# Kernel tuning notes

Hardware: AMD Instinct MI355X
Metric: run time of the kernel (lower is better)

The kernel has to match this reference:

```python
import jax, jax.numpy as jnp
import numpy as np

N = 8192
IN_DIM = 256
OUT_DIM = 256  # out_dim//num_heads * num_heads == out_dim
EDGE_PROB = 0.01


def setup_inputs() -> dict:
    key = jax.random.key(0)
    k_adj, k_h, k_q, k_k, k_v = jax.random.split(key, 5)
    # Dense 0/1 adjacency mask, multiplied into the score matrix.
    adj = (jax.random.uniform(k_adj, (N, N)) < EDGE_PROB).astype(jnp.float32)
    h = jax.random.normal(k_h, (N, IN_DIM), dtype=jnp.float32)
    # torch nn.Linear stores weight as [out_features, in_features]; no bias (use_bias=False).
    s = 1.0 / np.sqrt(IN_DIM)
    Wq = jax.random.normal(k_q, (OUT_DIM, IN_DIM), dtype=jnp.float32) * s
    Wk = jax.random.normal(k_k, (OUT_DIM, IN_DIM), dtype=jnp.float32) * s
    Wv = jax.random.normal(k_v, (OUT_DIM, IN_DIM), dtype=jnp.float32) * s
    return {"adj": adj, "h": h, "Wq": Wq, "Wk": Wk, "Wv": Wv}


def reference(adj, h, Wq, Wk, Wv):
    # Q_h, K_h, V_h: [N, out_dim]
    Q_h = h @ Wq.T
    K_h = h @ Wk.T
    V_h = h @ Wv.T
    scale = 1.0 / jnp.sqrt(jnp.asarray(h.shape[1], dtype=h.dtype))
    # Scores masked multiplicatively by adjacency (faithful to source: zeros,
    # not -inf, so non-edges still contribute exp(0) after softmax).
    A_tilde = scale * (Q_h @ K_h.T) * adj            # [N, N]
    attention = jax.nn.softmax(A_tilde, axis=1)       # softmax over dim 1
    X_tilde = attention @ V_h                         # [N, out_dim]
    return X_tilde
```

## Files before the change

### kernel.cpp

```cpp
#include <hip/hip_runtime.h>


#define NN  8192
#define DIM 256
#define SCALE 0.0625f
#define CAP 32

typedef __attribute__((ext_vector_type(8))) short short8;
typedef __attribute__((ext_vector_type(4))) float f32x4;
typedef __attribute__((ext_vector_type(4))) unsigned int u32x4;
typedef __attribute__((ext_vector_type(4))) unsigned short u16x4;

__device__ __forceinline__ unsigned short f2bf(float f) {
    union { float f; unsigned u; } v; v.f = f;
    unsigned u = v.u;
    unsigned r = (u + 0x7fffu + ((u >> 16) & 1u)) >> 16;
    return (unsigned short)r;
}
__device__ __forceinline__ float bf2f(unsigned short s) {
    union { unsigned u; float f; } v; v.u = ((unsigned)s) << 16;
    return v.f;
}
__device__ __forceinline__ float dw_lo(unsigned u) {
    union { unsigned u; float f; } v; v.u = u << 16; return v.f;
}
__device__ __forceinline__ float dw_hi(unsigned u) {
    union { unsigned u; float f; } v; v.u = u & 0xffff0000u; return v.f;
}

__global__ __launch_bounds__(256) void prep_kernel(
    const float* __restrict__ h, const float* __restrict__ Wq,
    const float* __restrict__ Wk, const float* __restrict__ Wv,
    unsigned short* __restrict__ h_bf, unsigned short* __restrict__ w_bf)
{
    int b = blockIdx.x, t = threadIdx.x;
    if (b < 2048) {
        int idx = (b * 256 + t) * 4;
        float4 v = *(const float4*)(h + idx);
        ushort4 o; o.x = f2bf(v.x); o.y = f2bf(v.y); o.z = f2bf(v.z); o.w = f2bf(v.w);
        *(ushort4*)(h_bf + idx) = o;
    } else {
        int idx = ((b - 2048) * 256 + t) * 4;
        int w = idx >> 16;
        int offn = idx & 65535;
        const float* src = (w == 0) ? Wq : (w == 1) ? Wk : Wv;
        float4 v = *(const float4*)(src + offn);
        ushort4 o; o.x = f2bf(v.x); o.y = f2bf(v.y); o.z = f2bf(v.z); o.w = f2bf(v.w);
        *(ushort4*)(w_bf + idx) = o;
    }
}

__global__ __launch_bounds__(256) void proj_gemm(
    const unsigned short* __restrict__ h_bf, const unsigned short* __restrict__ w_bf,
    float* __restrict__ Q, unsigned short* __restrict__ Kb, unsigned short* __restrict__ Vb)
{
    __shared__ unsigned short sB[256][40];
    const int mb = blockIdx.x, p = blockIdx.y;
    const unsigned short* W = w_bf + (p << 16);
    const int tid = threadIdx.x, wave = tid >> 6, lane = tid & 63;

    f32x4 acc[16];
#pragma unroll
    for (int f = 0; f < 16; ++f) acc[f] = (f32x4)(0.0f);

    const int arow = mb * 64 + wave * 16 + (lane & 15);
    const int ko   = (lane >> 4) * 8;

    for (int kk = 0; kk < 256; kk += 32) {
        __syncthreads();
        {
            const uint4* src = (const uint4*)(W + tid * 256 + kk);
            uint4* dst = (uint4*)(&sB[tid][0]);
            dst[0] = src[0]; dst[1] = src[1]; dst[2] = src[2]; dst[3] = src[3];
        }
        __syncthreads();
        short8 a = *(const short8*)(h_bf + (size_t)arow * 256 + kk + ko);
#pragma unroll
        for (int f = 0; f < 16; ++f) {
            short8 b = *(const short8*)(&sB[f * 16 + (lane & 15)][ko]);
            acc[f] = __builtin_amdgcn_mfma_f32_16x16x32_bf16(a, b, acc[f], 0, 0, 0);
        }
    }

    const int orow = mb * 64 + wave * 16 + ((lane >> 4) << 2);
    const int ocol = lane & 15;
    if (p == 0) {
#pragma unroll
        for (int f = 0; f < 16; ++f)
#pragma unroll
            for (int r = 0; r < 4; ++r)
                Q[(size_t)(orow + r) * 256 + f * 16 + ocol] = acc[f][r];
    } else {
        unsigned short* dstb = (p == 1) ? Kb : Vb;
#pragma unroll
        for (int f = 0; f < 16; ++f)
#pragma unroll
            for (int r = 0; r < 4; ++r)
                dstb[(size_t)(orow + r) * 256 + f * 16 + ocol] = f2bf(acc[f][r]);
    }
}

__global__ __launch_bounds__(256) void vsum_partial(
    const unsigned short* __restrict__ Vb, float* __restrict__ partial)
{
    int b = blockIdx.x, t = threadIdx.x;
    float s = 0.0f;
    for (int r = 0; r < 64; ++r)
        s += bf2f(Vb[(size_t)(b * 64 + r) * 256 + t]);
    partial[b * 256 + t] = s;
}
__global__ __launch_bounds__(256) void vsum_final(
    const float* __restrict__ partial, float* __restrict__ Vsum)
{
    int t = threadIdx.x;
    float s = 0.0f;
    for (int b = 0; b < 128; ++b) s += partial[b * 256 + t];
    Vsum[t] = s;
}

__global__ __launch_bounds__(128) void attn_e(
    const float* __restrict__ adj, const float* __restrict__ Q,
    const unsigned short* __restrict__ Kb, const unsigned short* __restrict__ Vb,
    unsigned short* __restrict__ pnum, float* __restrict__ pden)
{
    __shared__ unsigned short s_idx[2][CAP];

    const int e    = blockIdx.x >> 12;
    const int i    = ((blockIdx.x & 4095) << 1) + (threadIdx.x >> 6);
    const int lane = threadIdx.x & 63;
    const int w    = threadIdx.x >> 6;
    const unsigned long long lt = (1ull << lane) - 1ull;

    const f32x4* arow4 = (const f32x4*)(adj + (size_t)i * NN + e * 1024);
    f32x4 a0 = __builtin_nontemporal_load(arow4 + lane);
    f32x4 a1 = __builtin_nontemporal_load(arow4 + 64 + lane);
    f32x4 a2 = __builtin_nontemporal_load(arow4 + 128 + lane);
    f32x4 a3 = __builtin_nontemporal_load(arow4 + 192 + lane);

    const float* Qi = Q + (size_t)i * DIM + (lane & 15) * 16;
    f32x4 q0 = *(const f32x4*)(Qi);
    f32x4 q1 = *(const f32x4*)(Qi + 4);
    f32x4 q2 = *(const f32x4*)(Qi + 8);
    f32x4 q3 = *(const f32x4*)(Qi + 12);

    const int jbase = e * 1024;
    int off = 0;
#pragma unroll
    for (int s = 0; s < 4; ++s) {
        f32x4 av = (s == 0) ? a0 : (s == 1) ? a1 : (s == 2) ? a2 : a3;
        const int colbase = jbase + (s * 64 + lane) * 4;
#pragma unroll
        for (int c = 0; c < 4; ++c) {
            bool nz = (av[c] != 0.0f);
            unsigned long long m = __ballot(nz);
            if (nz) {
                int pos = off + __popcll(m & lt);
                if (pos < CAP) s_idx[w][pos] = (unsigned short)(colbase + c);
            }
            off += __popcll(m);
        }
    }
    const int cnt = (off < CAP) ? off : CAP;

    const int g = lane >> 4;
    float acc0 = 0.f, acc1 = 0.f, acc2 = 0.f, acc3 = 0.f, den = 0.f;
    const int rounds = (cnt + 3) >> 2;

#pragma unroll 2
    for (int r = 0; r < rounds; ++r) {
        const int kb0 = r * 4;
        int jg0 = (kb0 + 0 < cnt) ? (int)s_idx[w][kb0 + 0] : 0;
        int jg1 = (kb0 + 1 < cnt) ? (int)s_idx[w][kb0 + 1] : 0;
        int jg2 = (kb0 + 2 < cnt) ? (int)s_idx[w][kb0 + 2] : 0;
        int jg3 = (kb0 + 3 < cnt) ? (int)s_idx[w][kb0 + 3] : 0;

        const bool myv = (kb0 + g) < cnt;
        const int  myj = (g == 0) ? jg0 : (g == 1) ? jg1 : (g == 2) ? jg2 : jg3;

        const u32x4* kp = (const u32x4*)(Kb + (size_t)myj * DIM + (lane & 15) * 16);
        u32x4 ka = kp[0];
        u32x4 kc = kp[1];

        ushort4 v0 = *(const ushort4*)(Vb + (size_t)jg0 * DIM + lane * 4);
        ushort4 v1 = *(const ushort4*)(Vb + (size_t)jg1 * DIM + lane * 4);
        ushort4 v2 = *(const ushort4*)(Vb + (size_t)jg2 * DIM + lane * 4);
        ushort4 v3 = *(const ushort4*)(Vb + (size_t)jg3 * DIM + lane * 4);

        float d0 = q0[0] * dw_lo(ka[0]);
        float d1 = q0[1] * dw_hi(ka[0]);
        float d2 = q0[2] * dw_lo(ka[1]);
        float d3 = q0[3] * dw_hi(ka[1]);
        d0 = fmaf(q1[0], dw_lo(ka[2]), d0);
        d1 = fmaf(q1[1], dw_hi(ka[2]), d1);
        d2 = fmaf(q1[2], dw_lo(ka[3]), d2);
        d3 = fmaf(q1[3], dw_hi(ka[3]), d3);
        d0 = fmaf(q2[0], dw_lo(kc[0]), d0);
        d1 = fmaf(q2[1], dw_hi(kc[0]), d1);
        d2 = fmaf(q2[2], dw_lo(kc[1]), d2);
        d3 = fmaf(q2[3], dw_hi(kc[1]), d3);
        d0 = fmaf(q3[0], dw_lo(kc[2]), d0);
        d1 = fmaf(q3[1], dw_hi(kc[2]), d1);
        d2 = fmaf(q3[2], dw_lo(kc[3]), d2);
        d3 = fmaf(q3[3], dw_hi(kc[3]), d3);
        float d = (d0 + d1) + (d2 + d3);

        d += __shfl_xor(d, 1);
        d += __shfl_xor(d, 2);
        d += __shfl_xor(d, 4);
        d += __shfl_xor(d, 8);

        float ev = myv ? (__expf(SCALE * d) - 1.0f) : 0.0f;

        float e0 = __shfl(ev, 0);
        float e1 = __shfl(ev, 16);
        float e2 = __shfl(ev, 32);
        float e3 = __shfl(ev, 48);
        den += (e0 + e1) + (e2 + e3);

        acc0 = fmaf(e0, bf2f(v0.x), acc0); acc1 = fmaf(e0, bf2f(v0.y), acc1);
        acc2 = fmaf(e0, bf2f(v0.z), acc2); acc3 = fmaf(e0, bf2f(v0.w), acc3);
        acc0 = fmaf(e1, bf2f(v1.x), acc0); acc1 = fmaf(e1, bf2f(v1.y), acc1);
        acc2 = fmaf(e1, bf2f(v1.z), acc2); acc3 = fmaf(e1, bf2f(v1.w), acc3);
        acc0 = fmaf(e2, bf2f(v2.x), acc0); acc1 = fmaf(e2, bf2f(v2.y), acc1);
        acc2 = fmaf(e2, bf2f(v2.z), acc2); acc3 = fmaf(e2, bf2f(v2.w), acc3);
        acc0 = fmaf(e3, bf2f(v3.x), acc0); acc1 = fmaf(e3, bf2f(v3.y), acc1);
        acc2 = fmaf(e3, bf2f(v3.z), acc2); acc3 = fmaf(e3, bf2f(v3.w), acc3);
    }

    u16x4 o = { f2bf(acc0), f2bf(acc1), f2bf(acc2), f2bf(acc3) };
    __builtin_nontemporal_store(o, (u16x4*)(pnum + ((size_t)i * 8 + e) * 256 + lane * 4));
    if (lane == 0) pden[(size_t)i * 8 + e] = den;
}

__global__ __launch_bounds__(256) void finalize(
    const unsigned short* __restrict__ pnum, const float* __restrict__ pden,
    const float* __restrict__ Vsum, float* __restrict__ out)
{
    const int i = blockIdx.x, t = threadIdx.x;
    float num = 0.0f, den = 0.0f;
#pragma unroll
    for (int x = 0; x < 8; ++x) {
        num += bf2f(pnum[((size_t)i * 8 + x) * 256 + t]);
        den += pden[(size_t)i * 8 + x];
    }
    out[(size_t)i * DIM + t] = (Vsum[t] + num) / (8192.0f + den);
}

extern "C" void kernel_launch(void* const* d_in, const int* in_sizes, int n_in,
                              void* d_out, int out_size, void* d_ws, size_t ws_size,
                              hipStream_t stream)
{
    const float* adj = (const float*)d_in[0];
    const float* h   = (const float*)d_in[1];
    const float* Wq  = (const float*)d_in[2];
    const float* Wk  = (const float*)d_in[3];
    const float* Wv  = (const float*)d_in[4];
    float* out = (float*)d_out;

    char* ws = (char*)d_ws;
    size_t off = 0;
    unsigned short* p_hbf = (unsigned short*)(ws + off); off += (size_t)NN * DIM * 2;
    unsigned short* p_wbf = (unsigned short*)(ws + off); off += (size_t)3 * DIM * DIM * 2;
    off = (off + 1023) & ~(size_t)1023;
    float*          p_Q   = (float*)(ws + off);          off += (size_t)NN * DIM * 4;
    unsigned short* p_Kb  = (unsigned short*)(ws + off); off += (size_t)NN * DIM * 2;
    unsigned short* p_Vb  = (unsigned short*)(ws + off); off += (size_t)NN * DIM * 2;
    float*          p_par = (float*)(ws + off);          off += (size_t)128 * DIM * 4;
    float*          p_vs  = (float*)(ws + off);          off += DIM * 4;
    unsigned short* p_pn  = (unsigned short*)(ws + off); off += (size_t)NN * 8 * 256 * 2;
    float*          p_pd  = (float*)(ws + off);          off += (size_t)NN * 8 * 4;
    (void)ws_size; (void)in_sizes; (void)n_in; (void)out_size;

    prep_kernel<<<2240, 256, 0, stream>>>(h, Wq, Wk, Wv, p_hbf, p_wbf);
    proj_gemm<<<dim3(128, 3), 256, 0, stream>>>(p_hbf, p_wbf, p_Q, p_Kb, p_Vb);
    vsum_partial<<<128, 256, 0, stream>>>(p_Vb, p_par);
    vsum_final<<<1, 256, 0, stream>>>(p_par, p_vs);
    attn_e<<<NN * 8 / 2, 128, 0, stream>>>(adj, p_Q, p_Kb, p_Vb, p_pn, p_pd);
    finalize<<<NN, 256, 0, stream>>>(p_pn, p_pd, p_vs, out);
}
```

Baseline: 131.8 us.

## Reassociate attention through h: fold Wq^T Wk and defer Wv projection

Rewrites the maths so scores come from (h·Wq^T·Wk)·h^T and the aggregation runs over raw h rows, applying Wv once after normalisation with a final GEMM. This removes the K and V projections and their storage, so the sparse gather loop reads only one bf16 row per neighbour instead of both K and V rows. The dot product now uses a full 64-lane shuffle reduction over 4 neighbours at once. The cost is two extra small kernels (the 256x256 M generation and the output GEMM), plus an extra bf16 rounding of the M product and the aggregated T matrix.

```diff
diff --git a/kernel.cpp b/kernel.cpp
--- a/kernel.cpp
+++ b/kernel.cpp
@@ -8,7 +8,6 @@
 
 typedef __attribute__((ext_vector_type(8))) short short8;
 typedef __attribute__((ext_vector_type(4))) float f32x4;
-typedef __attribute__((ext_vector_type(4))) unsigned int u32x4;
 typedef __attribute__((ext_vector_type(4))) unsigned short u16x4;
 
 __device__ __forceinline__ unsigned short f2bf(float f) {
@@ -20,12 +19,6 @@
 __device__ __forceinline__ float bf2f(unsigned short s) {
     union { unsigned u; float f; } v; v.u = ((unsigned)s) << 16;
     return v.f;
-}
-__device__ __forceinline__ float dw_lo(unsigned u) {
-    union { unsigned u; float f; } v; v.u = u << 16; return v.f;
-}
-__device__ __forceinline__ float dw_hi(unsigned u) {
-    union { unsigned u; float f; } v; v.u = u & 0xffff0000u; return v.f;
 }
 
 __global__ __launch_bounds__(256) void prep_kernel(
@@ -50,13 +43,26 @@
     }
 }
 
-__global__ __launch_bounds__(256) void proj_gemm(
-    const unsigned short* __restrict__ h_bf, const unsigned short* __restrict__ w_bf,
-    float* __restrict__ Q, unsigned short* __restrict__ Kb, unsigned short* __restrict__ Vb)
+__global__ __launch_bounds__(256) void mgen(
+    const unsigned short* __restrict__ w_bf, unsigned short* __restrict__ Mt)
+{
+    __shared__ float s_col[256];
+    const int a = blockIdx.x, t = threadIdx.x;
+    s_col[t] = bf2f(w_bf[t * 256 + a]);
+    __syncthreads();
+    const unsigned short* Wk = w_bf + 65536;
+    float acc = 0.f;
+    for (int o = 0; o < 256; ++o)
+        acc = fmaf(s_col[o], bf2f(Wk[o * 256 + t]), acc);
+    Mt[(size_t)t * 256 + a] = f2bf(acc);
+}
+
+__global__ __launch_bounds__(256) void gemm_q(
+    const unsigned short* __restrict__ A, const unsigned short* __restrict__ B,
+    float* __restrict__ C)
 {
     __shared__ unsigned short sB[256][40];
-    const int mb = blockIdx.x, p = blockIdx.y;
-    const unsigned short* W = w_bf + (p << 16);
+    const int mb = blockIdx.x;
     const int tid = threadIdx.x, wave = tid >> 6, lane = tid & 63;
 
     f32x4 acc[16];
@@ -69,12 +75,12 @@
     for (int kk = 0; kk < 256; kk += 32) {
         __syncthreads();
         {
-            const uint4* src = (const uint4*)(W + tid * 256 + kk);
+            const uint4* src = (const uint4*)(B + tid * 256 + kk);
             uint4* dst = (uint4*)(&sB[tid][0]);
             dst[0] = src[0]; dst[1] = src[1]; dst[2] = src[2]; dst[3] = src[3];
         }
         __syncthreads();
-        short8 a = *(const short8*)(h_bf + (size_t)arow * 256 + kk + ko);
+        short8 a = *(const short8*)(A + (size_t)arow * 256 + kk + ko);
 #pragma unroll
         for (int f = 0; f < 16; ++f) {
             short8 b = *(const short8*)(&sB[f * 16 + (lane & 15)][ko]);
@@ -84,43 +90,78 @@
 
     const int orow = mb * 64 + wave * 16 + ((lane >> 4) << 2);
     const int ocol = lane & 15;
-    if (p == 0) {
-#pragma unroll
-        for (int f = 0; f < 16; ++f)
-#pragma unroll
-            for (int r = 0; r < 4; ++r)
-                Q[(size_t)(orow + r) * 256 + f * 16 + ocol] = acc[f][r];
-    } else {
-        unsigned short* dstb = (p == 1) ? Kb : Vb;
-#pragma unroll
-        for (int f = 0; f < 16; ++f)
-#pragma unroll
-            for (int r = 0; r < 4; ++r)
-                dstb[(size_t)(orow + r) * 256 + f * 16 + ocol] = f2bf(acc[f][r]);
-    }
-}
-
-__global__ __launch_bounds__(256) void vsum_partial(
-    const unsigned short* __restrict__ Vb, float* __restrict__ partial)
+#pragma unroll
+    for (int f = 0; f < 16; ++f)
+#pragma unroll
+        for (int r = 0; r < 4; ++r)
+            C[(size_t)(orow + r) * 256 + f * 16 + ocol] = acc[f][r];
+}
+
+__global__ __launch_bounds__(256) void gemm_out(
+    const unsigned short* __restrict__ Tb, const unsigned short* __restrict__ Wv,
+    const float* __restrict__ dfac, float* __restrict__ out)
+{
+    __shared__ unsigned short sB[256][40];
+    const int mb = blockIdx.x;
+    const int tid = threadIdx.x, wave = tid >> 6, lane = tid & 63;
+
+    f32x4 acc[16];
+#pragma unroll
+    for (int f = 0; f < 16; ++f) acc[f] = (f32x4)(0.0f);
+
+    const int arow = mb * 64 + wave * 16 + (lane & 15);
+    const int ko   = (lane >> 4) * 8;
+
+    for (int kk = 0; kk < 256; kk += 32) {
+        __syncthreads();
+        {
+            const uint4* src = (const uint4*)(Wv + tid * 256 + kk);
+            uint4* dst = (uint4*)(&sB[tid][0]);
+            dst[0] = src[0]; dst[1] = src[1]; dst[2] = src[2]; dst[3] = src[3];
+        }
+        __syncthreads();
+        short8 a = *(const short8*)(Tb + (size_t)arow * 256 + kk + ko);
+#pragma unroll
+        for (int f = 0; f < 16; ++f) {
+            short8 b = *(const short8*)(&sB[f * 16 + (lane & 15)][ko]);
+            acc[f] = __builtin_amdgcn_mfma_f32_16x16x32_bf16(a, b, acc[f], 0, 0, 0);
+        }
+    }
+
+    const int orow = mb * 64 + wave * 16 + ((lane >> 4) << 2);
+    const int ocol = lane & 15;
+    float df0 = dfac[orow + 0], df1 = dfac[orow + 1];
+    float df2 = dfac[orow + 2], df3 = dfac[orow + 3];
+#pragma unroll
+    for (int f = 0; f < 16; ++f) {
+        out[(size_t)(orow + 0) * 256 + f * 16 + ocol] = acc[f][0] * df0;
+        out[(size_t)(orow + 1) * 256 + f * 16 + ocol] = acc[f][1] * df1;
+        out[(size_t)(orow + 2) * 256 + f * 16 + ocol] = acc[f][2] * df2;
+        out[(size_t)(orow + 3) * 256 + f * 16 + ocol] = acc[f][3] * df3;
+    }
+}
+
+__global__ __launch_bounds__(256) void hsum_partial(
+    const unsigned short* __restrict__ hb, float* __restrict__ partial)
 {
     int b = blockIdx.x, t = threadIdx.x;
     float s = 0.0f;
     for (int r = 0; r < 64; ++r)
-        s += bf2f(Vb[(size_t)(b * 64 + r) * 256 + t]);
+        s += bf2f(hb[(size_t)(b * 64 + r) * 256 + t]);
     partial[b * 256 + t] = s;
 }
-__global__ __launch_bounds__(256) void vsum_final(
-    const float* __restrict__ partial, float* __restrict__ Vsum)
+__global__ __launch_bounds__(256) void hsum_final(
+    const float* __restrict__ partial, float* __restrict__ hsum)
 {
     int t = threadIdx.x;
     float s = 0.0f;
     for (int b = 0; b < 128; ++b) s += partial[b * 256 + t];
-    Vsum[t] = s;
+    hsum[t] = s;
 }
 
 __global__ __launch_bounds__(128) void attn_e(
     const float* __restrict__ adj, const float* __restrict__ Q,
-    const unsigned short* __restrict__ Kb, const unsigned short* __restrict__ Vb,
+    const unsigned short* __restrict__ hb,
     unsigned short* __restrict__ pnum, float* __restrict__ pden)
 {
     __shared__ unsigned short s_idx[2][CAP];
@@ -137,11 +178,7 @@
     f32x4 a2 = __builtin_nontemporal_load(arow4 + 128 + lane);
     f32x4 a3 = __builtin_nontemporal_load(arow4 + 192 + lane);
 
-    const float* Qi = Q + (size_t)i * DIM + (lane & 15) * 16;
-    f32x4 q0 = *(const f32x4*)(Qi);
-    f32x4 q1 = *(const f32x4*)(Qi + 4);
-    f32x4 q2 = *(const f32x4*)(Qi + 8);
-    f32x4 q3 = *(const f32x4*)(Qi + 12);
+    f32x4 q = *(const f32x4*)(Q + (size_t)i * DIM + lane * 4);
 
     const int jbase = e * 1024;
     int off = 0;
@@ -162,7 +199,6 @@
     }
     const int cnt = (off < CAP) ? off : CAP;
 
-    const int g = lane >> 4;
     float acc0 = 0.f, acc1 = 0.f, acc2 = 0.f, acc3 = 0.f, den = 0.f;
     const int rounds = (cnt + 3) >> 2;
 
@@ -174,57 +210,43 @@
         int jg2 = (kb0 + 2 < cnt) ? (int)s_idx[w][kb0 + 2] : 0;
         int jg3 = (kb0 + 3 < cnt) ? (int)s_idx[w][kb0 + 3] : 0;
 
-        const bool myv = (kb0 + g) < cnt;
-        const int  myj = (g == 0) ? jg0 : (g == 1) ? jg1 : (g == 2) ? jg2 : jg3;
-
-        const u32x4* kp = (const u32x4*)(Kb + (size_t)myj * DIM + (lane & 15) * 16);
-        u32x4 ka = kp[0];
-        u32x4 kc = kp[1];
-
-        ushort4 v0 = *(const ushort4*)(Vb + (size_t)jg0 * DIM + lane * 4);
-        ushort4 v1 = *(const ushort4*)(Vb + (size_t)jg1 * DIM + lane * 4);
-        ushort4 v2 = *(const ushort4*)(Vb + (size_t)jg2 * DIM + lane * 4);
-        ushort4 v3 = *(const ushort4*)(Vb + (size_t)jg3 * DIM + lane * 4);
-
-        float d0 = q0[0] * dw_lo(ka[0]);
-        float d1 = q0[1] * dw_hi(ka[0]);
-        float d2 = q0[2] * dw_lo(ka[1]);
-        float d3 = q0[3] * dw_hi(ka[1]);
-        d0 = fmaf(q1[0], dw_lo(ka[2]), d0);
-        d1 = fmaf(q1[1], dw_hi(ka[2]), d1);
-        d2 = fmaf(q1[2], dw_lo(ka[3]), d2);
-        d3 = fmaf(q1[3], dw_hi(ka[3]), d3);
-        d0 = fmaf(q2[0], dw_lo(kc[0]), d0);
-        d1 = fmaf(q2[1], dw_hi(kc[0]), d1);
-        d2 = fmaf(q2[2], dw_lo(kc[1]), d2);
-        d3 = fmaf(q2[3], dw_hi(kc[1]), d3);
-        d0 = fmaf(q3[0], dw_lo(kc[2]), d0);
-        d1 = fmaf(q3[1], dw_hi(kc[2]), d1);
-        d2 = fmaf(q3[2], dw_lo(kc[3]), d2);
-        d3 = fmaf(q3[3], dw_hi(kc[3]), d3);
-        float d = (d0 + d1) + (d2 + d3);
-
-        d += __shfl_xor(d, 1);
-        d += __shfl_xor(d, 2);
-        d += __shfl_xor(d, 4);
-        d += __shfl_xor(d, 8);
-
-        float ev = myv ? (__expf(SCALE * d) - 1.0f) : 0.0f;
-
-        float e0 = __shfl(ev, 0);
-        float e1 = __shfl(ev, 16);
-        float e2 = __shfl(ev, 32);
-        float e3 = __shfl(ev, 48);
+        ushort4 v0 = *(const ushort4*)(hb + (size_t)jg0 * DIM + lane * 4);
+        ushort4 v1 = *(const ushort4*)(hb + (size_t)jg1 * DIM + lane * 4);
+        ushort4 v2 = *(const ushort4*)(hb + (size_t)jg2 * DIM + lane * 4);
+        ushort4 v3 = *(const ushort4*)(hb + (size_t)jg3 * DIM + lane * 4);
+
+        float f00 = bf2f(v0.x), f01 = bf2f(v0.y), f02 = bf2f(v0.z), f03 = bf2f(v0.w);
+        float f10 = bf2f(v1.x), f11 = bf2f(v1.y), f12 = bf2f(v1.z), f13 = bf2f(v1.w);
+        float f20 = bf2f(v2.x), f21 = bf2f(v2.y), f22 = bf2f(v2.z), f23 = bf2f(v2.w);
+        float f30 = bf2f(v3.x), f31 = bf2f(v3.y), f32_ = bf2f(v3.z), f33 = bf2f(v3.w);
+
+        float d0 = q[0] * f00; d0 = fmaf(q[1], f01, d0); d0 = fmaf(q[2], f02, d0); d0 = fmaf(q[3], f03, d0);
+        float d1 = q[0] * f10; d1 = fmaf(q[1], f11, d1); d1 = fmaf(q[2], f12, d1); d1 = fmaf(q[3], f13, d1);
+        float d2 = q[0] * f20; d2 = fmaf(q[1], f21, d2); d2 = fmaf(q[2], f22, d2); d2 = fmaf(q[3], f23, d2);
+        float d3 = q[0] * f30; d3 = fmaf(q[1], f31, d3); d3 = fmaf(q[2], f32_, d3); d3 = fmaf(q[3], f33, d3);
+
+#pragma unroll
+        for (int m = 1; m < 64; m <<= 1) {
+            d0 += __shfl_xor(d0, m);
+            d1 += __shfl_xor(d1, m);
+            d2 += __shfl_xor(d2, m);
+            d3 += __shfl_xor(d3, m);
+        }
+
+        float e0 = (kb0 + 0 < cnt) ? (__expf(SCALE * d0) - 1.0f) : 0.0f;
+        float e1 = (kb0 + 1 < cnt) ? (__expf(SCALE * d1) - 1.0f) : 0.0f;
+        float e2 = (kb0 + 2 < cnt) ? (__expf(SCALE * d2) - 1.0f) : 0.0f;
+        float e3 = (kb0 + 3 < cnt) ? (__expf(SCALE * d3) - 1.0f) : 0.0f;
         den += (e0 + e1) + (e2 + e3);
 
-        acc0 = fmaf(e0, bf2f(v0.x), acc0); acc1 = fmaf(e0, bf2f(v0.y), acc1);
-        acc2 = fmaf(e0, bf2f(v0.z), acc2); acc3 = fmaf(e0, bf2f(v0.w), acc3);
-        acc0 = fmaf(e1, bf2f(v1.x), acc0); acc1 = fmaf(e1, bf2f(v1.y), acc1);
-        acc2 = fmaf(e1, bf2f(v1.z), acc2); acc3 = fmaf(e1, bf2f(v1.w), acc3);
-        acc0 = fmaf(e2, bf2f(v2.x), acc0); acc1 = fmaf(e2, bf2f(v2.y), acc1);
-        acc2 = fmaf(e2, bf2f(v2.z), acc2); acc3 = fmaf(e2, bf2f(v2.w), acc3);
-        acc0 = fmaf(e3, bf2f(v3.x), acc0); acc1 = fmaf(e3, bf2f(v3.y), acc1);
-        acc2 = fmaf(e3, bf2f(v3.z), acc2); acc3 = fmaf(e3, bf2f(v3.w), acc3);
+        acc0 = fmaf(e0, f00, acc0); acc1 = fmaf(e0, f01, acc1);
+        acc2 = fmaf(e0, f02, acc2); acc3 = fmaf(e0, f03, acc3);
+        acc0 = fmaf(e1, f10, acc0); acc1 = fmaf(e1, f11, acc1);
+        acc2 = fmaf(e1, f12, acc2); acc3 = fmaf(e1, f13, acc3);
+        acc0 = fmaf(e2, f20, acc0); acc1 = fmaf(e2, f21, acc1);
+        acc2 = fmaf(e2, f22, acc2); acc3 = fmaf(e2, f23, acc3);
+        acc0 = fmaf(e3, f30, acc0); acc1 = fmaf(e3, f31, acc1);
+        acc2 = fmaf(e3, f32_, acc2); acc3 = fmaf(e3, f33, acc3);
     }
 
     u16x4 o = { f2bf(acc0), f2bf(acc1), f2bf(acc2), f2bf(acc3) };
@@ -232,18 +254,20 @@
     if (lane == 0) pden[(size_t)i * 8 + e] = den;
 }
 
-__global__ __launch_bounds__(256) void finalize(
+__global__ __launch_bounds__(256) void tfinal(
     const unsigned short* __restrict__ pnum, const float* __restrict__ pden,
-    const float* __restrict__ Vsum, float* __restrict__ out)
+    const float* __restrict__ hsum, unsigned short* __restrict__ Tb,
+    float* __restrict__ dfac)
 {
     const int i = blockIdx.x, t = threadIdx.x;
-    float num = 0.0f, den = 0.0f;
+    float num = hsum[t], den = 0.0f;
 #pragma unroll
     for (int x = 0; x < 8; ++x) {
         num += bf2f(pnum[((size_t)i * 8 + x) * 256 + t]);
         den += pden[(size_t)i * 8 + x];
     }
-    out[(size_t)i * DIM + t] = (Vsum[t] + num) / (8192.0f + den);
+    Tb[(size_t)i * 256 + t] = f2bf(num);
+    if (t == 0) dfac[i] = 1.0f / (8192.0f + den);
 }
 
 extern "C" void kernel_launch(void* const* d_in, const int* in_sizes, int n_in,
@@ -262,19 +286,22 @@
     unsigned short* p_hbf = (unsigned short*)(ws + off); off += (size_t)NN * DIM * 2;
     unsigned short* p_wbf = (unsigned short*)(ws + off); off += (size_t)3 * DIM * DIM * 2;
     off = (off + 1023) & ~(size_t)1023;
+    unsigned short* p_Mt  = (unsigned short*)(ws + off); off += (size_t)DIM * DIM * 2;
     float*          p_Q   = (float*)(ws + off);          off += (size_t)NN * DIM * 4;
-    unsigned short* p_Kb  = (unsigned short*)(ws + off); off += (size_t)NN * DIM * 2;
-    unsigned short* p_Vb  = (unsigned short*)(ws + off); off += (size_t)NN * DIM * 2;
     float*          p_par = (float*)(ws + off);          off += (size_t)128 * DIM * 4;
-    float*          p_vs  = (float*)(ws + off);          off += DIM * 4;
+    float*          p_hs  = (float*)(ws + off);          off += DIM * 4;
     unsigned short* p_pn  = (unsigned short*)(ws + off); off += (size_t)NN * 8 * 256 * 2;
     float*          p_pd  = (float*)(ws + off);          off += (size_t)NN * 8 * 4;
+    unsigned short* p_Tb  = (unsigned short*)(ws + off); off += (size_t)NN * DIM * 2;
+    float*          p_df  = (float*)(ws + off);          off += (size_t)NN * 4;
     (void)ws_size; (void)in_sizes; (void)n_in; (void)out_size;
 
     prep_kernel<<<2240, 256, 0, stream>>>(h, Wq, Wk, Wv, p_hbf, p_wbf);
-    proj_gemm<<<dim3(128, 3), 256, 0, stream>>>(p_hbf, p_wbf, p_Q, p_Kb, p_Vb);
-    vsum_partial<<<128, 256, 0, stream>>>(p_Vb, p_par);
-    vsum_final<<<1, 256, 0, stream>>>(p_par, p_vs);
-    attn_e<<<NN * 8 / 2, 128, 0, stream>>>(adj, p_Q, p_Kb, p_Vb, p_pn, p_pd);
-    finalize<<<NN, 256, 0, stream>>>(p_pn, p_pd, p_vs, out);
-}
+    mgen<<<256, 256, 0, stream>>>(p_wbf, p_Mt);
+    gemm_q<<<128, 256, 0, stream>>>(p_hbf, p_Mt, p_Q);
+    hsum_partial<<<128, 256, 0, stream>>>(p_hbf, p_par);
+    hsum_final<<<1, 256, 0, stream>>>(p_par, p_hs);
+    attn_e<<<NN * 8 / 2, 128, 0, stream>>>(adj, p_Q, p_hbf, p_pn, p_pd);
+    tfinal<<<NN, 256, 0, stream>>>(p_pn, p_pd, p_hs, p_Tb, p_df);
+    gemm_out<<<128, 256, 0, stream>>>(p_Tb, p_wbf + 2 * 65536, p_df, out);
+}
```

After: 136.7 us. +3.7%, slower.
